# Kernel optimization log

Hardware: AMD Instinct MI355X
Metric: run time of the kernel (lower is better)

## Reference

```python
import jax, jax.numpy as jnp
import numpy as np

N = 50000; E = 800000; G = 256; F = 34; D = 128; H = 4; C = 32; L = 4
EPS = 1e-5

def _bn(x, g, b):
    # BatchNorm1d with batch statistics (train-mode math), eval dropout (identity)
    m = jnp.mean(x, 0); v = jnp.var(x, 0)
    return g * (x - m) * jax.lax.rsqrt(v + EPS) + b

def _seg_softmax(s, seg, n):
    # numerically-stable softmax over edges grouped by destination node
    m = jax.ops.segment_max(s, seg, num_segments=n)
    m = jnp.where(jnp.isfinite(m), m, 0.0)
    e = jnp.exp(s - m[seg])
    d = jax.ops.segment_sum(e, seg, num_segments=n)
    return e / (d[seg] + 1e-16)

def setup_inputs():
    key = jax.random.key(0)
    ks = iter(jax.random.split(key, 64))
    def rn(shape, s=0.05):
        return jax.random.normal(next(ks), shape, dtype=jnp.float32) * s
    inp = {}
    inp['x'] = jax.random.normal(next(ks), (N, F), dtype=jnp.float32)
    inp['edge_index'] = jax.random.randint(next(ks), (2, E), 0, N, dtype=jnp.int32)
    inp['batch'] = jnp.sort(jax.random.randint(next(ks), (N,), 0, G, dtype=jnp.int32))
    inp['emb_W'] = rn((F, D)); inp['emb_b'] = rn((D,))
    inp['emb_g'] = jnp.ones((D,)); inp['emb_be'] = jnp.zeros((D,))
    inp['gWl'] = rn((L, D, D)); inp['gWr'] = rn((L, D, D))
    inp['gbl'] = rn((L, D)); inp['gbr'] = rn((L, D))
    inp['gatt'] = rn((L, H, C)); inp['gbias'] = rn((L, D))
    inp['gg'] = jnp.ones((L, D)); inp['gbe'] = jnp.zeros((L, D))
    inp['tWq'] = rn((D, D)); inp['tWk'] = rn((D, D)); inp['tWv'] = rn((D, D)); inp['tWs'] = rn((D, D))
    inp['tbq'] = rn((D,)); inp['tbk'] = rn((D,)); inp['tbv'] = rn((D,)); inp['tbs'] = rn((D,))
    inp['tg'] = jnp.ones((D,)); inp['tbe'] = jnp.zeros((D,))
    inp['oW1'] = rn((2 * D, D)); inp['ob1'] = rn((D,))
    inp['og'] = jnp.ones((D,)); inp['obe'] = jnp.zeros((D,))
    inp['oW2'] = rn((D, D // 2)); inp['ob2'] = rn((D // 2,))
    inp['oW3'] = rn((D // 2, 1)); inp['ob3'] = rn((1,))
    return inp

def reference(x, edge_index, batch, emb_W, emb_b, emb_g, emb_be, gWl, gWr, gbl, gbr, gatt, gbias, gg, gbe, tWq, tWk, tWv, tWs, tbq, tbk, tbv, tbs, tg, tbe, oW1, ob1, og, obe, oW2, ob2, oW3, ob3):
    x = jax.nn.relu(_bn(x @ emb_W + emb_b, emb_g, emb_be))
    sl = jnp.arange(N, dtype=edge_index.dtype)
    ei = jnp.concatenate([edge_index, jnp.stack([sl, sl])], axis=1)  # GATv2 default add_self_loops=True
    src, dst = ei[0], ei[1]
    for l in range(L):  # 4 structurally identical GATv2 layers
        xl = (x @ gWl[l] + gbl[l]).reshape(N, H, C)
        xr = (x @ gWr[l] + gbr[l]).reshape(N, H, C)
        e = jax.nn.leaky_relu(xl[src] + xr[dst], 0.2)  # [E+N, H, C]
        sc = jnp.einsum('ehc,hc->eh', e, gatt[l])
        a = _seg_softmax(sc, dst, N)
        out = jax.ops.segment_sum(xl[src] * a[..., None], dst, num_segments=N).reshape(N, D) + gbias[l]
        x = x + jax.nn.relu(_bn(out, gg[l], gbe[l]))
    # TransformerConv: no self-loops by default, dot-product attention + root skip
    s2, d2 = edge_index[0], edge_index[1]
    q = (x @ tWq + tbq).reshape(N, H, C)
    k = (x @ tWk + tbk).reshape(N, H, C)
    v = (x @ tWv + tbv).reshape(N, H, C)
    sc = jnp.einsum('ehc,ehc->eh', q[d2], k[s2]) / np.float32(np.sqrt(C))
    a = _seg_softmax(sc, d2, N)
    agg = jax.ops.segment_sum(v[s2] * a[..., None], d2, num_segments=N).reshape(N, D)
    x = x + _bn(agg + x @ tWs + tbs, tg, tbe)
    # global mean + max pooling over graphs
    cnt = jax.ops.segment_sum(jnp.ones((N,), x.dtype), batch, num_segments=G)
    xm = jax.ops.segment_sum(x, batch, num_segments=G) / jnp.maximum(cnt, 1.0)[:, None]
    xx = jax.ops.segment_max(x, batch, num_segments=G)
    xx = jnp.where(jnp.isfinite(xx), xx, 0.0)  # guard empty segments
    h = jnp.concatenate([xm, xx], axis=1)
    h = jax.nn.relu(_bn(h @ oW1 + ob1, og, obe))
    h = jax.nn.relu(h @ oW2 + ob2)
    return h @ oW3 + ob3
```

## Files before the change

### kernel.cpp

```cpp
#include <hip/hip_runtime.h>
#include <hip/hip_fp16.h>

namespace {
constexpr int NN = 50000;
constexpr int NE = 800000;
constexpr int NG = 256;
constexpr int NF = 34;
constexpr int NL = 4;
constexpr int NB = (NN + 255) / 256;
constexpr int STS = 32;
}
#define EPSB 1e-5f
#define LSLOPE 0.2f
#define INV_SQRT_C 0.17677669529663687f

typedef short bf16x8 __attribute__((ext_vector_type(8)));
typedef float f32x4 __attribute__((ext_vector_type(4)));
typedef _Float16 hv2 __attribute__((ext_vector_type(2)));

static __device__ __forceinline__ short f2bf(float f) {
    unsigned int u = __float_as_uint(f);
    u = (u + 0x7fff + ((u >> 16) & 1)) >> 16;
    return (short)u;
}
static __device__ __forceinline__ unsigned fenc(float x) {
    unsigned u = __float_as_uint(x);
    return (u & 0x80000000u) ? ~u : (u | 0x80000000u);
}
static __device__ __forceinline__ float fdec(unsigned u) {
    return __uint_as_float((u & 0x80000000u) ? (u ^ 0x80000000u) : ~u);
}
static __device__ __forceinline__ float fdot2(hv2 a, hv2 b, float c) {
    return __builtin_amdgcn_fdot2(a, b, c, false);
}

__global__ __launch_bounds__(256) void k_deg(const int* __restrict__ ei,
                                             int* __restrict__ deg,
                                             int* __restrict__ rank) {
    int tid = blockIdx.x * 256 + threadIdx.x;
    const int S = (NE + 3) / 4;
    if (tid >= S) return;
#pragma unroll
    for (int k = 0; k < 4; ++k) {
        int e = tid + k * S;
        if (e < NE) rank[e] = atomicAdd(&deg[ei[NE + e]], 1);
    }
}

__global__ __launch_bounds__(256) void k_scan1(const int* __restrict__ deg, int* __restrict__ bsum) {
    __shared__ int sm[256];
    int i = blockIdx.x * 256 + threadIdx.x;
    sm[threadIdx.x] = (i < NN) ? deg[i] : 0;
    __syncthreads();
    for (int off = 128; off > 0; off >>= 1) {
        if (threadIdx.x < off) sm[threadIdx.x] += sm[threadIdx.x + off];
        __syncthreads();
    }
    if (threadIdx.x == 0) bsum[blockIdx.x] = sm[0];
}

__global__ __launch_bounds__(256) void k_scan2(const int* __restrict__ bsum,
                                               int* __restrict__ boff, int* __restrict__ rp) {
    __shared__ int sm[256];
    int t = threadIdx.x;
    int v = (t < NB) ? bsum[t] : 0;
    sm[t] = v;
    __syncthreads();
    for (int off = 1; off < 256; off <<= 1) {
        int u = (t >= off) ? sm[t - off] : 0;
        __syncthreads();
        sm[t] += u;
        __syncthreads();
    }
    if (t < NB) boff[t] = sm[t] - v;
    if (t == 255) rp[NN] = sm[255];
}

__global__ __launch_bounds__(256) void k_scan3(const int* __restrict__ deg,
                                               const int* __restrict__ boff,
                                               int* __restrict__ rp) {
    __shared__ int sm[256];
    int i = blockIdx.x * 256 + threadIdx.x;
    int t = threadIdx.x;
    int v = (i < NN) ? deg[i] : 0;
    sm[t] = v;
    __syncthreads();
    for (int off = 1; off < 256; off <<= 1) {
        int u = (t >= off) ? sm[t - off] : 0;
        __syncthreads();
        sm[t] += u;
        __syncthreads();
    }
    if (i < NN) rp[i] = boff[blockIdx.x] + sm[t] - v;
}

__global__ __launch_bounds__(256) void k_fill(const int* __restrict__ ei,
                                              const int* __restrict__ rp,
                                              const int* __restrict__ rank,
                                              int* __restrict__ esrc) {
    int tid = blockIdx.x * 256 + threadIdx.x;
    const int S = (NE + 3) / 4;
    if (tid >= S) return;
#pragma unroll
    for (int k = 0; k < 4; ++k) {
        int e = tid + k * S;
        if (e < NE) {
            int s = ei[e];
            int d = ei[NE + e];
            int p = rp[d] + rank[e];
            esrc[p] = s;
        }
    }
}

__global__ __launch_bounds__(256) void k_prep(const float* __restrict__ gWl,
                                              const float* __restrict__ gWr,
                                              const float* __restrict__ tWq,
                                              const float* __restrict__ tWk,
                                              const float* __restrict__ tWv,
                                              const float* __restrict__ tWs,
                                              short* __restrict__ dst) {
    int m = blockIdx.x;
    const float* src;
    if (m < 4) src = gWl + m * 16384;
    else if (m < 8) src = gWr + (m - 4) * 16384;
    else if (m == 8) src = tWq;
    else if (m == 9) src = tWk;
    else if (m == 10) src = tWv;
    else src = tWs;
    short* d = dst + m * 16384;
    for (int i = threadIdx.x; i < 16384; i += 256) {
        int n = i >> 7, k = i & 127;
        d[i] = f2bf(src[k * 128 + n]);
    }
}

template <int OUTH0, int OUTH1, int RES, int XOUT>
__global__ __launch_bounds__(256) void k_gemm2bn(const float* __restrict__ src,
                                                 const float* __restrict__ res,
                                                 float* __restrict__ xout,
                                                 const float* __restrict__ st,
                                                 const float* __restrict__ g,
                                                 const float* __restrict__ b,
                                                 const short* __restrict__ Wt0,
                                                 const short* __restrict__ Wt1,
                                                 const float* __restrict__ bias0,
                                                 const float* __restrict__ bias1,
                                                 void* __restrict__ out0,
                                                 void* __restrict__ out1, int nRows) {
    __shared__ short As[128 * 136];
    __shared__ short Bs[128 * 136];
    __shared__ float scsh[256];
    const float invn = 1.f / NN;
    if (threadIdx.x < 128) {
        int c = threadIdx.x;
        float s0v = 0.f, s1v = 0.f;
#pragma unroll 8
        for (int k2 = 0; k2 < STS; ++k2) {
            s0v += st[k2 * 256 + c];
            s1v += st[k2 * 256 + 128 + c];
        }
        float mean = s0v * invn;
        float var = fmaxf(s1v * invn - mean * mean, 0.f);
        float s = g[c] * rsqrtf(var + EPSB);
        scsh[c] = s;
        scsh[128 + c] = b[c] - mean * s;
    }
    {
        const int4* Wt4 = (const int4*)Wt0;
        for (int idx = threadIdx.x; idx < 2048; idx += 256) {
            int row = idx >> 4, c8 = idx & 15;
            *(int4*)&Bs[row * 136 + c8 * 8] = Wt4[idx];
        }
    }
    __syncthreads();
    int r0 = blockIdx.x * 128;
    int rows = nRows - r0; if (rows > 128) rows = 128;
    for (int idx = threadIdx.x; idx < 2048; idx += 256) {
        int r = idx >> 4, c8 = idx & 15;
        short4 sa = {0, 0, 0, 0}, sb = {0, 0, 0, 0};
        if (r < rows) {
            size_t base = (size_t)(r0 + r) * 128 + c8 * 8;
            float4 v0 = *(const float4*)&src[base];
            float4 v1 = *(const float4*)&src[base + 4];
            int c = c8 * 8;
            v0.x = fmaxf(v0.x * scsh[c + 0] + scsh[128 + c + 0], 0.f);
            v0.y = fmaxf(v0.y * scsh[c + 1] + scsh[128 + c + 1], 0.f);
            v0.z = fmaxf(v0.z * scsh[c + 2] + scsh[128 + c + 2], 0.f);
            v0.w = fmaxf(v0.w * scsh[c + 3] + scsh[128 + c + 3], 0.f);
            v1.x = fmaxf(v1.x * scsh[c + 4] + scsh[128 + c + 4], 0.f);
            v1.y = fmaxf(v1.y * scsh[c + 5] + scsh[128 + c + 5], 0.f);
            v1.z = fmaxf(v1.z * scsh[c + 6] + scsh[128 + c + 6], 0.f);
            v1.w = fmaxf(v1.w * scsh[c + 7] + scsh[128 + c + 7], 0.f);
            if (RES) {
                float4 rr0 = *(const float4*)&res[base];
                float4 rr1 = *(const float4*)&res[base + 4];
                v0.x += rr0.x; v0.y += rr0.y; v0.z += rr0.z; v0.w += rr0.w;
                v1.x += rr1.x; v1.y += rr1.y; v1.z += rr1.z; v1.w += rr1.w;
            }
            if (XOUT) {
                *(float4*)&xout[base] = v0;
                *(float4*)&xout[base + 4] = v1;
            }
            sa.x = f2bf(v0.x); sa.y = f2bf(v0.y); sa.z = f2bf(v0.z); sa.w = f2bf(v0.w);
            sb.x = f2bf(v1.x); sb.y = f2bf(v1.y); sb.z = f2bf(v1.z); sb.w = f2bf(v1.w);
        }
        *(short4*)&As[r * 136 + c8 * 8] = sa;
        *(short4*)&As[r * 136 + c8 * 8 + 4] = sb;
    }
    __syncthreads();
    int lane = threadIdx.x & 63, wave = threadIdx.x >> 6;
    int n16 = lane & 15, quad = lane >> 4;
    bf16x8 af[2][4];
#pragma unroll
    for (int rt = 0; rt < 2; ++rt)
#pragma unroll
        for (int kc = 0; kc < 4; ++kc)
            af[rt][kc] = *(const bf16x8*)&As[(wave * 32 + rt * 16 + n16) * 136 + kc * 32 + quad * 8];

    f32x4 acc[2][8];
#pragma unroll
    for (int rt = 0; rt < 2; ++rt)
#pragma unroll
        for (int ct = 0; ct < 8; ++ct) acc[rt][ct] = (f32x4){0.f, 0.f, 0.f, 0.f};
#pragma unroll
    for (int ct = 0; ct < 8; ++ct)
#pragma unroll
        for (int kc = 0; kc < 4; ++kc) {
            bf16x8 bf = *(const bf16x8*)&Bs[(ct * 16 + n16) * 136 + kc * 32 + quad * 8];
            acc[0][ct] = __builtin_amdgcn_mfma_f32_16x16x32_bf16(af[0][kc], bf, acc[0][ct], 0, 0, 0);
            acc[1][ct] = __builtin_amdgcn_mfma_f32_16x16x32_bf16(af[1][kc], bf, acc[1][ct], 0, 0, 0);
        }
#pragma unroll
    for (int ct = 0; ct < 8; ++ct) {
        int colI = ct * 16 + n16;
        float bv = bias0[colI];
#pragma unroll
        for (int rt = 0; rt < 2; ++rt)
#pragma unroll
            for (int reg = 0; reg < 4; ++reg) {
                int r = wave * 32 + rt * 16 + quad * 4 + reg;
                if (r < rows) {
                    float v = acc[rt][ct][reg] + bv;
                    if (OUTH0) ((__half*)out0)[(size_t)(r0 + r) * 128 + colI] = __float2half(v);
                    else       ((float*)out0)[(size_t)(r0 + r) * 128 + colI] = v;
                }
            }
    }
    __syncthreads();
    {
        const int4* Wt4 = (const int4*)Wt1;
        for (int idx = threadIdx.x; idx < 2048; idx += 256) {
            int row = idx >> 4, c8 = idx & 15;
            *(int4*)&Bs[row * 136 + c8 * 8] = Wt4[idx];
        }
    }
    __syncthreads();
#pragma unroll
    for (int rt = 0; rt < 2; ++rt)
#pragma unroll
        for (int ct = 0; ct < 8; ++ct) acc[rt][ct] = (f32x4){0.f, 0.f, 0.f, 0.f};
#pragma unroll
    for (int ct = 0; ct < 8; ++ct)
#pragma unroll
        for (int kc = 0; kc < 4; ++kc) {
            bf16x8 bf = *(const bf16x8*)&Bs[(ct * 16 + n16) * 136 + kc * 32 + quad * 8];
            acc[0][ct] = __builtin_amdgcn_mfma_f32_16x16x32_bf16(af[0][kc], bf, acc[0][ct], 0, 0, 0);
            acc[1][ct] = __builtin_amdgcn_mfma_f32_16x16x32_bf16(af[1][kc], bf, acc[1][ct], 0, 0, 0);
        }
#pragma unroll
    for (int ct = 0; ct < 8; ++ct) {
        int colI = ct * 16 + n16;
        float bv = bias1[colI];
#pragma unroll
        for (int rt = 0; rt < 2; ++rt)
#pragma unroll
            for (int reg = 0; reg < 4; ++reg) {
                int r = wave * 32 + rt * 16 + quad * 4 + reg;
                if (r < rows) {
                    float v = acc[rt][ct][reg] + bv;
                    if (OUTH1) ((__half*)out1)[(size_t)(r0 + r) * 128 + colI] = __float2half(v);
                    else       ((float*)out1)[(size_t)(r0 + r) * 128 + colI] = v;
                }
            }
    }
}

__global__ __launch_bounds__(256) void k_gemm4bn(const float* __restrict__ src,
                                                 const float* __restrict__ res,
                                                 float* __restrict__ xout,
                                                 const float* __restrict__ st,
                                                 const float* __restrict__ g,
                                                 const float* __restrict__ b,
                                                 const short* __restrict__ Wt,
                                                 const float* __restrict__ bq,
                                                 const float* __restrict__ bk,
                                                 const float* __restrict__ bv,
                                                 const float* __restrict__ bs,
                                                 __half* __restrict__ oq,
                                                 __half* __restrict__ ok,
                                                 __half* __restrict__ ov,
                                                 __half* __restrict__ os, int nRows) {
    __shared__ short As[128 * 136];
    __shared__ short Bs[128 * 136];
    __shared__ float scsh[256];
    const float invn = 1.f / NN;
    if (threadIdx.x < 128) {
        int c = threadIdx.x;
        float s0v = 0.f, s1v = 0.f;
#pragma unroll 8
        for (int k2 = 0; k2 < STS; ++k2) {
            s0v += st[k2 * 256 + c];
            s1v += st[k2 * 256 + 128 + c];
        }
        float mean = s0v * invn;
        float var = fmaxf(s1v * invn - mean * mean, 0.f);
        float s = g[c] * rsqrtf(var + EPSB);
        scsh[c] = s;
        scsh[128 + c] = b[c] - mean * s;
    }
    __syncthreads();
    int r0 = blockIdx.x * 128;
    int rows = nRows - r0; if (rows > 128) rows = 128;
    for (int idx = threadIdx.x; idx < 2048; idx += 256) {
        int r = idx >> 4, c8 = idx & 15;
        short4 sa = {0, 0, 0, 0}, sb = {0, 0, 0, 0};
        if (r < rows) {
            size_t base = (size_t)(r0 + r) * 128 + c8 * 8;
            float4 v0 = *(const float4*)&src[base];
            float4 v1 = *(const float4*)&src[base + 4];
            int c = c8 * 8;
            v0.x = fmaxf(v0.x * scsh[c + 0] + scsh[128 + c + 0], 0.f);
            v0.y = fmaxf(v0.y * scsh[c + 1] + scsh[128 + c + 1], 0.f);
            v0.z = fmaxf(v0.z * scsh[c + 2] + scsh[128 + c + 2], 0.f);
            v0.w = fmaxf(v0.w * scsh[c + 3] + scsh[128 + c + 3], 0.f);
            v1.x = fmaxf(v1.x * scsh[c + 4] + scsh[128 + c + 4], 0.f);
            v1.y = fmaxf(v1.y * scsh[c + 5] + scsh[128 + c + 5], 0.f);
            v1.z = fmaxf(v1.z * scsh[c + 6] + scsh[128 + c + 6], 0.f);
            v1.w = fmaxf(v1.w * scsh[c + 7] + scsh[128 + c + 7], 0.f);
            float4 rr0 = *(const float4*)&res[base];
            float4 rr1 = *(const float4*)&res[base + 4];
            v0.x += rr0.x; v0.y += rr0.y; v0.z += rr0.z; v0.w += rr0.w;
            v1.x += rr1.x; v1.y += rr1.y; v1.z += rr1.z; v1.w += rr1.w;
            *(float4*)&xout[base] = v0;
            *(float4*)&xout[base + 4] = v1;
            sa.x = f2bf(v0.x); sa.y = f2bf(v0.y); sa.z = f2bf(v0.z); sa.w = f2bf(v0.w);
            sb.x = f2bf(v1.x); sb.y = f2bf(v1.y); sb.z = f2bf(v1.z); sb.w = f2bf(v1.w);
        }
        *(short4*)&As[r * 136 + c8 * 8] = sa;
        *(short4*)&As[r * 136 + c8 * 8 + 4] = sb;
    }
    int lane = threadIdx.x & 63, wave = threadIdx.x >> 6;
    int n16 = lane & 15, quad = lane >> 4;
    __half* outs[4] = {oq, ok, ov, os};
    const float* biases[4] = {bq, bk, bv, bs};
    bf16x8 af[2][4];
    bool afLoaded = false;
    for (int m = 0; m < 4; ++m) {
        {
            const int4* Wt4 = (const int4*)(Wt + (size_t)m * 16384);
            for (int idx = threadIdx.x; idx < 2048; idx += 256) {
                int row = idx >> 4, c8 = idx & 15;
                *(int4*)&Bs[row * 136 + c8 * 8] = Wt4[idx];
            }
        }
        __syncthreads();
        if (!afLoaded) {
            afLoaded = true;
#pragma unroll
            for (int rt = 0; rt < 2; ++rt)
#pragma unroll
                for (int kc = 0; kc < 4; ++kc)
                    af[rt][kc] = *(const bf16x8*)&As[(wave * 32 + rt * 16 + n16) * 136 + kc * 32 + quad * 8];
        }
        f32x4 acc[2][8];
#pragma unroll
        for (int rt = 0; rt < 2; ++rt)
#pragma unroll
            for (int ct = 0; ct < 8; ++ct) acc[rt][ct] = (f32x4){0.f, 0.f, 0.f, 0.f};
#pragma unroll
        for (int ct = 0; ct < 8; ++ct)
#pragma unroll
            for (int kc = 0; kc < 4; ++kc) {
                bf16x8 bf = *(const bf16x8*)&Bs[(ct * 16 + n16) * 136 + kc * 32 + quad * 8];
                acc[0][ct] = __builtin_amdgcn_mfma_f32_16x16x32_bf16(af[0][kc], bf, acc[0][ct], 0, 0, 0);
                acc[1][ct] = __builtin_amdgcn_mfma_f32_16x16x32_bf16(af[1][kc], bf, acc[1][ct], 0, 0, 0);
            }
        __half* om = outs[m];
        const float* bm = biases[m];
#pragma unroll
        for (int ct = 0; ct < 8; ++ct) {
            int colI = ct * 16 + n16;
            float bv2 = bm[colI];
#pragma unroll
            for (int rt = 0; rt < 2; ++rt)
#pragma unroll
                for (int reg = 0; reg < 4; ++reg) {
                    int r = wave * 32 + rt * 16 + quad * 4 + reg;
                    if (r < rows)
                        om[(size_t)(r0 + r) * 128 + colI] = __float2half(acc[rt][ct][reg] + bv2);
                }
        }
        if (m < 3) __syncthreads();
    }
}

__global__ __launch_bounds__(256) void k_gemm_emb(const float* __restrict__ A,
                                                  const float* __restrict__ W,
                                                  const float* __restrict__ bias,
                                                  float* __restrict__ out, int nRows,
                                                  float* __restrict__ stms) {
    __shared__ float As[64 * NF];
    __shared__ float sred[256];
    int r0 = blockIdx.x * 64;
    int rows = nRows - r0; if (rows > 64) rows = 64;
    int total = rows * NF;
    for (int idx = threadIdx.x; idx < 64 * NF; idx += 256)
        As[idx] = (idx < total) ? A[(size_t)r0 * NF + idx] : 0.f;
    sred[threadIdx.x] = 0.f;
    __syncthreads();
    int tx = threadIdx.x & 31, ty = threadIdx.x >> 5;
    const float4* W4 = (const float4*)W;
    float acc[8][4];
#pragma unroll
    for (int j = 0; j < 8; ++j)
#pragma unroll
        for (int i = 0; i < 4; ++i) acc[j][i] = 0.f;
#pragma unroll 2
    for (int k = 0; k < NF; ++k) {
        float4 w = W4[k * 32 + tx];
#pragma unroll
        for (int j = 0; j < 8; ++j) {
            float a = As[(ty * 8 + j) * NF + k];
            acc[j][0] += a * w.x; acc[j][1] += a * w.y;
            acc[j][2] += a * w.z; acc[j][3] += a * w.w;
        }
    }
    float4 b = ((const float4*)bias)[tx];
    float s[4] = {0.f, 0.f, 0.f, 0.f}, ss[4] = {0.f, 0.f, 0.f, 0.f};
#pragma unroll
    for (int j = 0; j < 8; ++j) {
        int r = ty * 8 + j;
        if (r < rows) {
            float4 o = make_float4(acc[j][0] + b.x, acc[j][1] + b.y,
                                   acc[j][2] + b.z, acc[j][3] + b.w);
            ((float4*)out)[(size_t)(r0 + r) * 32 + tx] = o;
            s[0] += o.x; ss[0] += o.x * o.x;
            s[1] += o.y; ss[1] += o.y * o.y;
            s[2] += o.z; ss[2] += o.z * o.z;
            s[3] += o.w; ss[3] += o.w * o.w;
        }
    }
#pragma unroll
    for (int i = 0; i < 4; ++i) {
        atomicAdd(&sred[tx * 4 + i], s[i]);
        atomicAdd(&sred[128 + tx * 4 + i], ss[i]);
    }
    __syncthreads();
    atomicAdd(&stms[(blockIdx.x & (STS - 1)) * 256 + threadIdx.x], sred[threadIdx.x]);
}

__global__ __launch_bounds__(256) void k_gat_aggr(const __half* __restrict__ xl,
                                                  const __half* __restrict__ xr,
                                                  const float* __restrict__ att,
                                                  const float* __restrict__ gbias_l,
                                                  const int* __restrict__ rp,
                                                  const int* __restrict__ esrc,
                                                  float* __restrict__ out,
                                                  float* __restrict__ stms) {
    __shared__ float smst[256];
    smst[threadIdx.x] = 0.f;
    __syncthreads();
    int lane = threadIdx.x & 63;
    int node = blockIdx.x * 4 + (threadIdx.x >> 6);
    int q = lane >> 4;
    int l16 = lane & 15;
    int c8 = l16 * 8;
    if (node < NN) {
        float4 xrr = *(const float4*)&xr[(unsigned)node * 128u + c8];
        hv2 xrv[4] = {*(hv2*)&xrr.x, *(hv2*)&xrr.y, *(hv2*)&xrr.z, *(hv2*)&xrr.w};
        float4 atA = *(const float4*)&att[c8];
        float4 atB = *(const float4*)&att[c8 + 4];
        hv2 ath[4] = {{(_Float16)atA.x, (_Float16)atA.y}, {(_Float16)atA.z, (_Float16)atA.w},
                      {(_Float16)atB.x, (_Float16)atB.y}, {(_Float16)atB.z, (_Float16)atB.w}};
        const hv2 hz = {(_Float16)0.f, (_Float16)0.f};
        const hv2 hs = {(_Float16)LSLOPE, (_Float16)LSLOPE};
        int s0 = rp[node];
        int T = rp[node + 1] - s0 + 1;
        float a[8] = {0.f, 0.f, 0.f, 0.f, 0.f, 0.f, 0.f, 0.f};
        float l = 0.f;
        auto body = [&](int j) {
            bool self = (j == T - 1);
            int srcn = self ? node : esrc[s0 + j];
            float4 raw = *(const float4*)&xl[(unsigned)srcn * 128u + c8];
            hv2 f[4] = {*(hv2*)&raw.x, *(hv2*)&raw.y, *(hv2*)&raw.z, *(hv2*)&raw.w};
            float p = 0.f;
#pragma unroll
            for (int k = 0; k < 4; ++k) {
                hv2 e = f[k] + xrv[k];
                hv2 lk = __builtin_elementwise_max(e, hz) + hs * __builtin_elementwise_min(e, hz);
                p = fdot2(lk, ath[k], p);
            }
            p += __shfl_xor(p, 1); p += __shfl_xor(p, 2);
            float w = __expf(p);
#pragma unroll
            for (int k = 0; k < 4; ++k) {
                a[2 * k] += w * (float)f[k].x;
                a[2 * k + 1] += w * (float)f[k].y;
            }
            l += w;
        };
        int j = q;
        for (; j + 4 < T; j += 8) { body(j); body(j + 4); }
        for (; j < T; j += 4) body(j);
#pragma unroll
        for (int k = 0; k < 8; ++k) { a[k] += __shfl_xor(a[k], 16); a[k] += __shfl_xor(a[k], 32); }
        l += __shfl_xor(l, 16); l += __shfl_xor(l, 32);
        if (q == 0) {
            float inv = 1.f / (l + 1e-16f);
            float4 gb0 = *(const float4*)&gbias_l[c8];
            float4 gb1 = *(const float4*)&gbias_l[c8 + 4];
            float o[8];
            o[0] = a[0] * inv + gb0.x; o[1] = a[1] * inv + gb0.y;
            o[2] = a[2] * inv + gb0.z; o[3] = a[3] * inv + gb0.w;
            o[4] = a[4] * inv + gb1.x; o[5] = a[5] * inv + gb1.y;
            o[6] = a[6] * inv + gb1.z; o[7] = a[7] * inv + gb1.w;
            *(float4*)&out[(unsigned)node * 128u + c8] = make_float4(o[0], o[1], o[2], o[3]);
            *(float4*)&out[(unsigned)node * 128u + c8 + 4] = make_float4(o[4], o[5], o[6], o[7]);
#pragma unroll
            for (int k = 0; k < 8; ++k) {
                atomicAdd(&smst[c8 + k], o[k]);
                atomicAdd(&smst[128 + c8 + k], o[k] * o[k]);
            }
        }
    }
    __syncthreads();
    atomicAdd(&stms[(blockIdx.x & (STS - 1)) * 256 + threadIdx.x], smst[threadIdx.x]);
}

__global__ __launch_bounds__(256) void k_trans_aggr(const __half* __restrict__ qh,
                                                    const __half* __restrict__ kh,
                                                    const __half* __restrict__ vv,
                                                    const __half* __restrict__ sT,
                                                    const int* __restrict__ rp,
                                                    const int* __restrict__ esrc,
                                                    float* __restrict__ out,
                                                    float* __restrict__ stms) {
    __shared__ float smst[256];
    smst[threadIdx.x] = 0.f;
    __syncthreads();
    int lane = threadIdx.x & 63;
    int node = blockIdx.x * 4 + (threadIdx.x >> 6);
    int q = lane >> 4;
    int l16 = lane & 15;
    int c8 = l16 * 8;
    if (node < NN) {
        float4 qr = *(const float4*)&qh[(unsigned)node * 128u + c8];
        const hv2 hinv = {(_Float16)INV_SQRT_C, (_Float16)INV_SQRT_C};
        hv2 qv[4] = {(*(hv2*)&qr.x) * hinv, (*(hv2*)&qr.y) * hinv,
                     (*(hv2*)&qr.z) * hinv, (*(hv2*)&qr.w) * hinv};
        int s0 = rp[node];
        int T = rp[node + 1] - s0;
        float a[8] = {0.f, 0.f, 0.f, 0.f, 0.f, 0.f, 0.f, 0.f};
        float l = 0.f;
        auto body = [&](int j) {
            int srcn = esrc[s0 + j];
            float4 kraw = *(const float4*)&kh[(unsigned)srcn * 128u + c8];
            float4 vraw = *(const float4*)&vv[(unsigned)srcn * 128u + c8];
            hv2 kv[4] = {*(hv2*)&kraw.x, *(hv2*)&kraw.y, *(hv2*)&kraw.z, *(hv2*)&kraw.w};
            float p = 0.f;
#pragma unroll
            for (int k = 0; k < 4; ++k) p = fdot2(kv[k], qv[k], p);
            p += __shfl_xor(p, 1); p += __shfl_xor(p, 2);
            float w = __expf(p);
            hv2 vvv[4] = {*(hv2*)&vraw.x, *(hv2*)&vraw.y, *(hv2*)&vraw.z, *(hv2*)&vraw.w};
#pragma unroll
            for (int k = 0; k < 4; ++k) {
                a[2 * k] += w * (float)vvv[k].x;
                a[2 * k + 1] += w * (float)vvv[k].y;
            }
            l += w;
        };
        int j = q;
        for (; j + 4 < T; j += 8) { body(j); body(j + 4); }
        for (; j < T; j += 4) body(j);
#pragma unroll
        for (int k = 0; k < 8; ++k) { a[k] += __shfl_xor(a[k], 16); a[k] += __shfl_xor(a[k], 32); }
        l += __shfl_xor(l, 16); l += __shfl_xor(l, 32);
        if (q == 0) {
            float inv = 1.f / (l + 1e-16f);
            float4 straw = *(const float4*)&sT[(unsigned)node * 128u + c8];
            hv2 st[4] = {*(hv2*)&straw.x, *(hv2*)&straw.y, *(hv2*)&straw.z, *(hv2*)&straw.w};
            float o[8];
            o[0] = a[0] * inv + (float)st[0].x; o[1] = a[1] * inv + (float)st[0].y;
            o[2] = a[2] * inv + (float)st[1].x; o[3] = a[3] * inv + (float)st[1].y;
            o[4] = a[4] * inv + (float)st[2].x; o[5] = a[5] * inv + (float)st[2].y;
            o[6] = a[6] * inv + (float)st[3].x; o[7] = a[7] * inv + (float)st[3].y;
            *(float4*)&out[(unsigned)node * 128u + c8] = make_float4(o[0], o[1], o[2], o[3]);
            *(float4*)&out[(unsigned)node * 128u + c8 + 4] = make_float4(o[4], o[5], o[6], o[7]);
#pragma unroll
            for (int k = 0; k < 8; ++k) {
                atomicAdd(&smst[c8 + k], o[k]);
                atomicAdd(&smst[128 + c8 + k], o[k] * o[k]);
            }
        }
    }
    __syncthreads();
    atomicAdd(&stms[(blockIdx.x & (STS - 1)) * 256 + threadIdx.x], smst[threadIdx.x]);
}

__global__ __launch_bounds__(256) void k_pool_part(const float* __restrict__ src,
                                                   const float* __restrict__ res,
                                                   const float* __restrict__ st,
                                                   const float* __restrict__ g,
                                                   const float* __restrict__ b,
                                                   const int* __restrict__ batch,
                                                   float* __restrict__ psum,
                                                   unsigned* __restrict__ pmax) {
    __shared__ int bs[64];
    __shared__ float sc_sh[128], sh_sh[128];
    int r0 = blockIdx.x * 64;
    if (threadIdx.x < 64) {
        int r = r0 + threadIdx.x;
        bs[threadIdx.x] = (r < NN) ? batch[r] : -1;
    }
    const float invn = 1.f / NN;
    if (threadIdx.x < 128) {
        int c2 = threadIdx.x;
        float s0v = 0.f, s1v = 0.f;
#pragma unroll 8
        for (int k2 = 0; k2 < STS; ++k2) {
            s0v += st[k2 * 256 + c2];
            s1v += st[k2 * 256 + 128 + c2];
        }
        float mean = s0v * invn;
        float var = fmaxf(s1v * invn - mean * mean, 0.f);
        float scv = g[c2] * rsqrtf(var + EPSB);
        sc_sh[c2] = scv;
        sh_sh[c2] = b[c2] - mean * scv;
    }
    __syncthreads();
    int c = threadIdx.x & 127;
    int sub = threadIdx.x >> 7;
    float scv = sc_sh[c];
    float shv = sh_sh[c];
    int curg = -1;
    float s = 0.f, fmx = -INFINITY;
    for (int i = sub; i < 64; i += 2) {
        int r = r0 + i;
        if (r >= NN) break;
        int gr = bs[i];
        if (gr != curg) {
            if (curg >= 0) {
                atomicAdd(&psum[curg * 128 + c], s);
                atomicMax(&pmax[curg * 128 + c], fenc(fmx));
            }
            curg = gr; s = 0.f; fmx = -INFINITY;
        }
        float v = src[(size_t)r * 128 + c] * scv + shv + res[(size_t)r * 128 + c];
        s += v; fmx = fmaxf(fmx, v);
    }
    if (curg >= 0) {
        atomicAdd(&psum[curg * 128 + c], s);
        atomicMax(&pmax[curg * 128 + c], fenc(fmx));
    }
}

__global__ __launch_bounds__(128) void k_pool_head1(const float* __restrict__ psum,
                                                    const unsigned* __restrict__ pmax,
                                                    const int* __restrict__ batch,
                                                    const float* __restrict__ W,
                                                    const float* __restrict__ b,
                                                    float* __restrict__ t1,
                                                    float* __restrict__ st6) {
    __shared__ float hr[256];
    __shared__ int se[2];
    int g = blockIdx.x;
    int t = threadIdx.x;
    if (t == 0) {
        int lo = 0, hi = NN;
        while (lo < hi) { int mid = (lo + hi) >> 1; if (batch[mid] < g) lo = mid + 1; else hi = mid; }
        se[0] = lo;
        hi = NN;
        while (lo < hi) { int mid = (lo + hi) >> 1; if (batch[mid] < g + 1) lo = mid + 1; else hi = mid; }
        se[1] = lo;
    }
    __syncthreads();
    int cnt = se[1] - se[0];
    float xm = psum[g * 128 + t] / fmaxf((float)cnt, 1.f);
    float xx = (cnt > 0) ? fdec(pmax[g * 128 + t]) : 0.f;
    hr[t] = xm;
    hr[128 + t] = xx;
    __syncthreads();
    float acc = b[t];
#pragma unroll 4
    for (int k = 0; k < 256; ++k) acc += hr[k] * W[k * 128 + t];
    t1[g * 128 + t] = acc;
    atomicAdd(&st6[t], acc);
    atomicAdd(&st6[128 + t], acc * acc);
}

__global__ __launch_bounds__(64) void k_head2(const float* __restrict__ t1,
                                              const float* __restrict__ st,
                                              const float* __restrict__ og,
                                              const float* __restrict__ obe,
                                              const float* __restrict__ W2,
                                              const float* __restrict__ b2,
                                              const float* __restrict__ W3,
                                              const float* __restrict__ b3,
                                              float* __restrict__ out) {
    __shared__ float v[128];
    int row = blockIdx.x, t = threadIdx.x;
    const float invn = 1.f / NG;
#pragma unroll
    for (int half = 0; half < 2; ++half) {
        int ch = t + half * 64;
        float mean = st[ch] * invn;
        float var = fmaxf(st[128 + ch] * invn - mean * mean, 0.f);
        float scv = og[ch] * rsqrtf(var + EPSB);
        float shv = obe[ch] - mean * scv;
        float a = t1[row * 128 + ch] * scv + shv;
        v[ch] = fmaxf(a, 0.f);
    }
    __syncthreads();
    float acc = b2[t];
#pragma unroll 4
    for (int k = 0; k < 128; ++k) acc += v[k] * W2[k * 64 + t];
    float p = fmaxf(acc, 0.f) * W3[t];
    p += __shfl_xor(p, 1); p += __shfl_xor(p, 2); p += __shfl_xor(p, 4);
    p += __shfl_xor(p, 8); p += __shfl_xor(p, 16); p += __shfl_xor(p, 32);
    if (t == 0) out[row] = p + b3[0];
}

extern "C" void kernel_launch(void* const* d_in, const int* in_sizes, int n_in,
                              void* d_out, int out_size, void* d_ws, size_t ws_size,
                              hipStream_t stream) {
    const float* x_in   = (const float*)d_in[0];
    const int*   ei     = (const int*)d_in[1];
    const int*   batch  = (const int*)d_in[2];
    const float* emb_W  = (const float*)d_in[3];
    const float* emb_b  = (const float*)d_in[4];
    const float* emb_g  = (const float*)d_in[5];
    const float* emb_be = (const float*)d_in[6];
    const float* gWl    = (const float*)d_in[7];
    const float* gWr    = (const float*)d_in[8];
    const float* gbl    = (const float*)d_in[9];
    const float* gbr    = (const float*)d_in[10];
    const float* gatt   = (const float*)d_in[11];
    const float* gbias  = (const float*)d_in[12];
    const float* gg     = (const float*)d_in[13];
    const float* gbe    = (const float*)d_in[14];
    const float* tWq    = (const float*)d_in[15];
    const float* tWk    = (const float*)d_in[16];
    const float* tWv    = (const float*)d_in[17];
    const float* tWs    = (const float*)d_in[18];
    const float* tbq    = (const float*)d_in[19];
    const float* tbk    = (const float*)d_in[20];
    const float* tbv    = (const float*)d_in[21];
    const float* tbs    = (const float*)d_in[22];
    const float* tg     = (const float*)d_in[23];
    const float* tbe    = (const float*)d_in[24];
    const float* oW1    = (const float*)d_in[25];
    const float* ob1    = (const float*)d_in[26];
    const float* og     = (const float*)d_in[27];
    const float* obe    = (const float*)d_in[28];
    const float* oW2    = (const float*)d_in[29];
    const float* ob2    = (const float*)d_in[30];
    const float* oW3    = (const float*)d_in[31];
    const float* ob3    = (const float*)d_in[32];
    float* out = (float*)d_out;

    const size_t NDsz = (size_t)NN * 128;
    float* x     = (float*)d_ws;
    float* bA    = x + NDsz;
    float* bC    = bA + NDsz;
    float* stats = bC + NDsz;
    float* hpool = stats + 7 * 256;
    float* t1    = hpool + 65536;
    float* scb   = t1 + 32768;
    __half* xlh  = (__half*)(scb + (size_t)(NE + NN) * 4);
    __half* xrh  = xlh + NDsz;
    __half* vh   = xrh + NDsz;
    __half* sh   = vh + NDsz;
    short* Wt    = (short*)(sh + NDsz);
    int* deg     = (int*)(Wt + 12 * 16384);
    int* rp      = deg + NN;
    int* cursor  = rp + NN + 1;
    int2* edg    = (int2*)(cursor + NN);
    int* bsum    = (int*)(edg + NE + 64);
    int* boff    = bsum + 256;
    float* psum  = (float*)(boff + 256);
    unsigned* pmax = (unsigned*)(psum + NG * 128);
    int* rank    = (int*)scb;
    int* esrc    = (int*)edg;
    float* stms  = scb + NE;

    hipMemsetAsync(deg, 0, NN * sizeof(int), stream);
    hipMemsetAsync(stats + 6 * 256, 0, 256 * sizeof(float), stream);
    hipMemsetAsync(stms, 0, 6 * STS * 256 * sizeof(float), stream);
    hipMemsetAsync(psum, 0, NG * 128 * 2 * sizeof(float), stream);

    k_prep<<<12, 256, 0, stream>>>(gWl, gWr, tWq, tWk, tWv, tWs, Wt);

    const int S4 = (NE + 3) / 4;
    const int gQuarter = (S4 + 255) / 256;
    k_deg<<<gQuarter, 256, 0, stream>>>(ei, deg, rank);
    k_scan1<<<NB, 256, 0, stream>>>(deg, bsum);
    k_scan2<<<1, 256, 0, stream>>>(bsum, boff, rp);
    k_scan3<<<NB, 256, 0, stream>>>(deg, boff, rp);
    k_fill<<<gQuarter, 256, 0, stream>>>(ei, rp, rank, esrc);

    const int gEmb  = (NN + 63) / 64;
    const int gGemm = (NN + 127) / 128;
    const int gNode = (NN + 3) / 4;
    const int gPool = (NN + 63) / 64;
    const int REG = STS * 256;

    k_gemm_emb<<<gEmb, 256, 0, stream>>>(x_in, emb_W, emb_b, bA, NN, stms + 0 * REG);

    k_gemm2bn<1, 1, 0, 1><<<gGemm, 256, 0, stream>>>(bA, nullptr, x, stms + 0 * REG, emb_g, emb_be,
                                                     Wt + (size_t)0 * 16384, Wt + (size_t)4 * 16384,
                                                     gbl + 0 * 128, gbr + 0 * 128, xlh, xrh, NN);
    k_gat_aggr<<<gNode, 256, 0, stream>>>(xlh, xrh, gatt + 0 * 128, gbias + 0 * 128, rp, esrc, bC, stms + 1 * REG);
    k_gemm2bn<1, 1, 1, 1><<<gGemm, 256, 0, stream>>>(bC, x, bA, stms + 1 * REG, gg + 0 * 128, gbe + 0 * 128,
                                                     Wt + (size_t)1 * 16384, Wt + (size_t)5 * 16384,
                                                     gbl + 1 * 128, gbr + 1 * 128, xlh, xrh, NN);
    k_gat_aggr<<<gNode, 256, 0, stream>>>(xlh, xrh, gatt + 1 * 128, gbias + 1 * 128, rp, esrc, bC, stms + 2 * REG);
    k_gemm2bn<1, 1, 1, 1><<<gGemm, 256, 0, stream>>>(bC, bA, x, stms + 2 * REG, gg + 1 * 128, gbe + 1 * 128,
                                                     Wt + (size_t)2 * 16384, Wt + (size_t)6 * 16384,
                                                     gbl + 2 * 128, gbr + 2 * 128, xlh, xrh, NN);
    k_gat_aggr<<<gNode, 256, 0, stream>>>(xlh, xrh, gatt + 2 * 128, gbias + 2 * 128, rp, esrc, bC, stms + 3 * REG);
    k_gemm2bn<1, 1, 1, 1><<<gGemm, 256, 0, stream>>>(bC, x, bA, stms + 3 * REG, gg + 2 * 128, gbe + 2 * 128,
                                                     Wt + (size_t)3 * 16384, Wt + (size_t)7 * 16384,
                                                     gbl + 3 * 128, gbr + 3 * 128, xlh, xrh, NN);
    k_gat_aggr<<<gNode, 256, 0, stream>>>(xlh, xrh, gatt + 3 * 128, gbias + 3 * 128, rp, esrc, bC, stms + 4 * REG);

    k_gemm4bn<<<gGemm, 256, 0, stream>>>(bC, bA, x, stms + 4 * REG, gg + 3 * 128, gbe + 3 * 128,
                                         Wt + (size_t)8 * 16384, tbq, tbk, tbv, tbs,
                                         xrh, xlh, vh, sh, NN);
    k_trans_aggr<<<gNode, 256, 0, stream>>>(xrh, xlh, vh, sh, rp, esrc, bC, stms + 5 * REG);

    k_pool_part<<<gPool, 256, 0, stream>>>(bC, x, stms + 5 * REG, tg, tbe, batch, psum, pmax);
    k_pool_head1<<<NG, 128, 0, stream>>>(psum, pmax, batch, oW1, ob1, t1, stats + 6 * 256);
    k_head2<<<NG, 64, 0, stream>>>(t1, stats + 6 * 256, og, obe, oW2, ob2, oW3, ob3, out);
}
```

Measured before the change: 935.4 us.

## Split BN statistics out of aggregation kernels into a separate stats pass

Removes the per-block shared-memory atomics and global stat accumulation from the GAT and Transformer aggregation kernels, letting waves exit early and dropping the block barrier. Column sums and sums of squares are instead computed by a new k_stats kernel that rereads the fp32 aggregation output. The gather loops are also unrolled by four instead of two to put more loads in flight. The trade is an extra 25.6 MB read plus one launch per layer against cheaper, barrier-free aggregation kernels.

```diff
diff --git a/kernel.cpp b/kernel.cpp
--- a/kernel.cpp
+++ b/kernel.cpp
@@ -133,6 +133,22 @@
         int n = i >> 7, k = i & 127;
         d[i] = f2bf(src[k * 128 + n]);
     }
+}
+
+__global__ __launch_bounds__(256) void k_stats(const float* __restrict__ src, int nRows,
+                                               float* __restrict__ st) {
+    int c = threadIdx.x & 127;
+    int sub = threadIdx.x >> 7;
+    int r0 = blockIdx.x * 128;
+    int rend = r0 + 128; if (rend > nRows) rend = nRows;
+    float s = 0.f, ss = 0.f;
+    for (int r = r0 + sub; r < rend; r += 2) {
+        float v = src[(size_t)r * 128 + c];
+        s += v; ss += v * v;
+    }
+    float* dst = st + (blockIdx.x & (STS - 1)) * 256;
+    atomicAdd(&dst[c], s);
+    atomicAdd(&dst[128 + c], ss);
 }
 
 template <int OUTH0, int OUTH1, int RES, int XOUT>
@@ -466,76 +482,64 @@
                                                   const float* __restrict__ gbias_l,
                                                   const int* __restrict__ rp,
                                                   const int* __restrict__ esrc,
-                                                  float* __restrict__ out,
-                                                  float* __restrict__ stms) {
-    __shared__ float smst[256];
-    smst[threadIdx.x] = 0.f;
-    __syncthreads();
+                                                  float* __restrict__ out) {
     int lane = threadIdx.x & 63;
     int node = blockIdx.x * 4 + (threadIdx.x >> 6);
+    if (node >= NN) return;
     int q = lane >> 4;
     int l16 = lane & 15;
     int c8 = l16 * 8;
-    if (node < NN) {
-        float4 xrr = *(const float4*)&xr[(unsigned)node * 128u + c8];
-        hv2 xrv[4] = {*(hv2*)&xrr.x, *(hv2*)&xrr.y, *(hv2*)&xrr.z, *(hv2*)&xrr.w};
-        float4 atA = *(const float4*)&att[c8];
-        float4 atB = *(const float4*)&att[c8 + 4];
-        hv2 ath[4] = {{(_Float16)atA.x, (_Float16)atA.y}, {(_Float16)atA.z, (_Float16)atA.w},
-                      {(_Float16)atB.x, (_Float16)atB.y}, {(_Float16)atB.z, (_Float16)atB.w}};
-        const hv2 hz = {(_Float16)0.f, (_Float16)0.f};
-        const hv2 hs = {(_Float16)LSLOPE, (_Float16)LSLOPE};
-        int s0 = rp[node];
-        int T = rp[node + 1] - s0 + 1;
-        float a[8] = {0.f, 0.f, 0.f, 0.f, 0.f, 0.f, 0.f, 0.f};
-        float l = 0.f;
-        auto body = [&](int j) {
-            bool self = (j == T - 1);
-            int srcn = self ? node : esrc[s0 + j];
-            float4 raw = *(const float4*)&xl[(unsigned)srcn * 128u + c8];
-            hv2 f[4] = {*(hv2*)&raw.x, *(hv2*)&raw.y, *(hv2*)&raw.z, *(hv2*)&raw.w};
-            float p = 0.f;
-#pragma unroll
-            for (int k = 0; k < 4; ++k) {
-                hv2 e = f[k] + xrv[k];
-                hv2 lk = __builtin_elementwise_max(e, hz) + hs * __builtin_elementwise_min(e, hz);
-                p = fdot2(lk, ath[k], p);
-            }
-            p += __shfl_xor(p, 1); p += __shfl_xor(p, 2);
-            float w = __expf(p);
-#pragma unroll
-            for (int k = 0; k < 4; ++k) {
-                a[2 * k] += w * (float)f[k].x;
-                a[2 * k + 1] += w * (float)f[k].y;
-            }
-            l += w;
-        };
-        int j = q;
-        for (; j + 4 < T; j += 8) { body(j); body(j + 4); }
-        for (; j < T; j += 4) body(j);
-#pragma unroll
-        for (int k = 0; k < 8; ++k) { a[k] += __shfl_xor(a[k], 16); a[k] += __shfl_xor(a[k], 32); }
-        l += __shfl_xor(l, 16); l += __shfl_xor(l, 32);
-        if (q == 0) {
-            float inv = 1.f / (l + 1e-16f);
-            float4 gb0 = *(const float4*)&gbias_l[c8];
-            float4 gb1 = *(const float4*)&gbias_l[c8 + 4];
-            float o[8];
-            o[0] = a[0] * inv + gb0.x; o[1] = a[1] * inv + gb0.y;
-            o[2] = a[2] * inv + gb0.z; o[3] = a[3] * inv + gb0.w;
-            o[4] = a[4] * inv + gb1.x; o[5] = a[5] * inv + gb1.y;
-            o[6] = a[6] * inv + gb1.z; o[7] = a[7] * inv + gb1.w;
-            *(float4*)&out[(unsigned)node * 128u + c8] = make_float4(o[0], o[1], o[2], o[3]);
-            *(float4*)&out[(unsigned)node * 128u + c8 + 4] = make_float4(o[4], o[5], o[6], o[7]);
-#pragma unroll
-            for (int k = 0; k < 8; ++k) {
-                atomicAdd(&smst[c8 + k], o[k]);
-                atomicAdd(&smst[128 + c8 + k], o[k] * o[k]);
-            }
-        }
-    }
-    __syncthreads();
-    atomicAdd(&stms[(blockIdx.x & (STS - 1)) * 256 + threadIdx.x], smst[threadIdx.x]);
+    float4 xrr = *(const float4*)&xr[(unsigned)node * 128u + c8];
+    hv2 xrh[4] = {*(hv2*)&xrr.x, *(hv2*)&xrr.y, *(hv2*)&xrr.z, *(hv2*)&xrr.w};
+    float4 atA = *(const float4*)&att[c8];
+    float4 atB = *(const float4*)&att[c8 + 4];
+    hv2 ath[4] = {{(_Float16)atA.x, (_Float16)atA.y}, {(_Float16)atA.z, (_Float16)atA.w},
+                  {(_Float16)atB.x, (_Float16)atB.y}, {(_Float16)atB.z, (_Float16)atB.w}};
+    const hv2 hz = {(_Float16)0.f, (_Float16)0.f};
+    const hv2 hs = {(_Float16)LSLOPE, (_Float16)LSLOPE};
+    int s0 = rp[node];
+    int T = rp[node + 1] - s0 + 1;
+    float a[8] = {0.f, 0.f, 0.f, 0.f, 0.f, 0.f, 0.f, 0.f};
+    float l = 0.f;
+    auto body = [&](int j) {
+        bool self = (j == T - 1);
+        int srcn = self ? node : esrc[s0 + j];
+        float4 raw = *(const float4*)&xl[(unsigned)srcn * 128u + c8];
+        hv2 f[4] = {*(hv2*)&raw.x, *(hv2*)&raw.y, *(hv2*)&raw.z, *(hv2*)&raw.w};
+        float p = 0.f;
+#pragma unroll
+        for (int k = 0; k < 4; ++k) {
+            hv2 e = f[k] + xrh[k];
+            hv2 lk = __builtin_elementwise_max(e, hz) + hs * __builtin_elementwise_min(e, hz);
+            p = fdot2(lk, ath[k], p);
+        }
+        p += __shfl_xor(p, 1); p += __shfl_xor(p, 2);
+        float w = __expf(p);
+#pragma unroll
+        for (int k = 0; k < 4; ++k) {
+            a[2 * k] += w * (float)f[k].x;
+            a[2 * k + 1] += w * (float)f[k].y;
+        }
+        l += w;
+    };
+    int j = q;
+    for (; j + 12 < T; j += 16) { body(j); body(j + 4); body(j + 8); body(j + 12); }
+    for (; j + 4 < T; j += 8) { body(j); body(j + 4); }
+    for (; j < T; j += 4) body(j);
+#pragma unroll
+    for (int k = 0; k < 8; ++k) { a[k] += __shfl_xor(a[k], 16); a[k] += __shfl_xor(a[k], 32); }
+    l += __shfl_xor(l, 16); l += __shfl_xor(l, 32);
+    if (q == 0) {
+        float inv = 1.f / (l + 1e-16f);
+        float4 gb0 = *(const float4*)&gbias_l[c8];
+        float4 gb1 = *(const float4*)&gbias_l[c8 + 4];
+        float4 o0 = make_float4(a[0] * inv + gb0.x, a[1] * inv + gb0.y,
+                                a[2] * inv + gb0.z, a[3] * inv + gb0.w);
+        float4 o1 = make_float4(a[4] * inv + gb1.x, a[5] * inv + gb1.y,
+                                a[6] * inv + gb1.z, a[7] * inv + gb1.w);
+        *(float4*)&out[(unsigned)node * 128u + c8] = o0;
+        *(float4*)&out[(unsigned)node * 128u + c8 + 4] = o1;
+    }
 }
 
 __global__ __launch_bounds__(256) void k_trans_aggr(const __half* __restrict__ qh,
@@ -544,69 +548,57 @@
                                                     const __half* __restrict__ sT,
                                                     const int* __restrict__ rp,
                                                     const int* __restrict__ esrc,
-                                                    float* __restrict__ out,
-                                                    float* __restrict__ stms) {
-    __shared__ float smst[256];
-    smst[threadIdx.x] = 0.f;
-    __syncthreads();
+                                                    float* __restrict__ out) {
     int lane = threadIdx.x & 63;
     int node = blockIdx.x * 4 + (threadIdx.x >> 6);
+    if (node >= NN) return;
     int q = lane >> 4;
     int l16 = lane & 15;
     int c8 = l16 * 8;
-    if (node < NN) {
-        float4 qr = *(const float4*)&qh[(unsigned)node * 128u + c8];
-        const hv2 hinv = {(_Float16)INV_SQRT_C, (_Float16)INV_SQRT_C};
-        hv2 qv[4] = {(*(hv2*)&qr.x) * hinv, (*(hv2*)&qr.y) * hinv,
-                     (*(hv2*)&qr.z) * hinv, (*(hv2*)&qr.w) * hinv};
-        int s0 = rp[node];
-        int T = rp[node + 1] - s0;
-        float a[8] = {0.f, 0.f, 0.f, 0.f, 0.f, 0.f, 0.f, 0.f};
-        float l = 0.f;
-        auto body = [&](int j) {
-            int srcn = esrc[s0 + j];
-            float4 kraw = *(const float4*)&kh[(unsigned)srcn * 128u + c8];
-            float4 vraw = *(const float4*)&vv[(unsigned)srcn * 128u + c8];
-            hv2 kv[4] = {*(hv2*)&kraw.x, *(hv2*)&kraw.y, *(hv2*)&kraw.z, *(hv2*)&kraw.w};
-            float p = 0.f;
-#pragma unroll
-            for (int k = 0; k < 4; ++k) p = fdot2(kv[k], qv[k], p);
-            p += __shfl_xor(p, 1); p += __shfl_xor(p, 2);
-            float w = __expf(p);
-            hv2 vvv[4] = {*(hv2*)&vraw.x, *(hv2*)&vraw.y, *(hv2*)&vraw.z, *(hv2*)&vraw.w};
-#pragma unroll
-            for (int k = 0; k < 4; ++k) {
-                a[2 * k] += w * (float)vvv[k].x;
-                a[2 * k + 1] += w * (float)vvv[k].y;
-            }
-            l += w;
-        };
-        int j = q;
-        for (; j + 4 < T; j += 8) { body(j); body(j + 4); }
-        for (; j < T; j += 4) body(j);
-#pragma unroll
-        for (int k = 0; k < 8; ++k) { a[k] += __shfl_xor(a[k], 16); a[k] += __shfl_xor(a[k], 32); }
-        l += __shfl_xor(l, 16); l += __shfl_xor(l, 32);
-        if (q == 0) {
-            float inv = 1.f / (l + 1e-16f);
-            float4 straw = *(const float4*)&sT[(unsigned)node * 128u + c8];
-            hv2 st[4] = {*(hv2*)&straw.x, *(hv2*)&straw.y, *(hv2*)&straw.z, *(hv2*)&straw.w};
-            float o[8];
-            o[0] = a[0] * inv + (float)st[0].x; o[1] = a[1] * inv + (float)st[0].y;
-            o[2] = a[2] * inv + (float)st[1].x; o[3] = a[3] * inv + (float)st[1].y;
-            o[4] = a[4] * inv + (float)st[2].x; o[5] = a[5] * inv + (float)st[2].y;
-            o[6] = a[6] * inv + (float)st[3].x; o[7] = a[7] * inv + (float)st[3].y;
-            *(float4*)&out[(unsigned)node * 128u + c8] = make_float4(o[0], o[1], o[2], o[3]);
-            *(float4*)&out[(unsigned)node * 128u + c8 + 4] = make_float4(o[4], o[5], o[6], o[7]);
-#pragma unroll
-            for (int k = 0; k < 8; ++k) {
-                atomicAdd(&smst[c8 + k], o[k]);
-                atomicAdd(&smst[128 + c8 + k], o[k] * o[k]);
-            }
-        }
-    }
-    __syncthreads();
-    atomicAdd(&stms[(blockIdx.x & (STS - 1)) * 256 + threadIdx.x], smst[threadIdx.x]);
+    float4 qr = *(const float4*)&qh[(unsigned)node * 128u + c8];
+    const hv2 hinv = {(_Float16)INV_SQRT_C, (_Float16)INV_SQRT_C};
+    hv2 qv[4] = {(*(hv2*)&qr.x) * hinv, (*(hv2*)&qr.y) * hinv,
+                 (*(hv2*)&qr.z) * hinv, (*(hv2*)&qr.w) * hinv};
+    int s0 = rp[node];
+    int T = rp[node + 1] - s0;
+    float a[8] = {0.f, 0.f, 0.f, 0.f, 0.f, 0.f, 0.f, 0.f};
+    float l = 0.f;
+    auto body = [&](int j) {
+        int srcn = esrc[s0 + j];
+        float4 kraw = *(const float4*)&kh[(unsigned)srcn * 128u + c8];
+        float4 vraw = *(const float4*)&vv[(unsigned)srcn * 128u + c8];
+        hv2 kv[4] = {*(hv2*)&kraw.x, *(hv2*)&kraw.y, *(hv2*)&kraw.z, *(hv2*)&kraw.w};
+        float p = 0.f;
+#pragma unroll
+        for (int k = 0; k < 4; ++k) p = fdot2(kv[k], qv[k], p);
+        p += __shfl_xor(p, 1); p += __shfl_xor(p, 2);
+        float w = __expf(p);
+        hv2 vvv[4] = {*(hv2*)&vraw.x, *(hv2*)&vraw.y, *(hv2*)&vraw.z, *(hv2*)&vraw.w};
+#pragma unroll
+        for (int k = 0; k < 4; ++k) {
+            a[2 * k] += w * (float)vvv[k].x;
+            a[2 * k + 1] += w * (float)vvv[k].y;
+        }
+        l += w;
+    };
+    int j = q;
+    for (; j + 12 < T; j += 16) { body(j); body(j + 4); body(j + 8); body(j + 12); }
+    for (; j + 4 < T; j += 8) { body(j); body(j + 4); }
+    for (; j < T; j += 4) body(j);
+#pragma unroll
+    for (int k = 0; k < 8; ++k) { a[k] += __shfl_xor(a[k], 16); a[k] += __shfl_xor(a[k], 32); }
+    l += __shfl_xor(l, 16); l += __shfl_xor(l, 32);
+    if (q == 0) {
+        float inv = 1.f / (l + 1e-16f);
+        float4 straw = *(const float4*)&sT[(unsigned)node * 128u + c8];
+        hv2 st[4] = {*(hv2*)&straw.x, *(hv2*)&straw.y, *(hv2*)&straw.z, *(hv2*)&straw.w};
+        float4 o0 = make_float4(a[0] * inv + (float)st[0].x, a[1] * inv + (float)st[0].y,
+                                a[2] * inv + (float)st[1].x, a[3] * inv + (float)st[1].y);
+        float4 o1 = make_float4(a[4] * inv + (float)st[2].x, a[5] * inv + (float)st[2].y,
+                                a[6] * inv + (float)st[3].x, a[7] * inv + (float)st[3].y);
+        *(float4*)&out[(unsigned)node * 128u + c8] = o0;
+        *(float4*)&out[(unsigned)node * 128u + c8 + 4] = o1;
+    }
 }
 
 __global__ __launch_bounds__(256) void k_pool_part(const float* __restrict__ src,
@@ -812,6 +804,7 @@
 
     const int gEmb  = (NN + 63) / 64;
     const int gGemm = (NN + 127) / 128;
+    const int gStat = (NN + 127) / 128;
     const int gNode = (NN + 3) / 4;
     const int gPool = (NN + 63) / 64;
     const int REG = STS * 256;
@@ -821,24 +814,29 @@
     k_gemm2bn<1, 1, 0, 1><<<gGemm, 256, 0, stream>>>(bA, nullptr, x, stms + 0 * REG, emb_g, emb_be,
                                                      Wt + (size_t)0 * 16384, Wt + (size_t)4 * 16384,
                                                      gbl + 0 * 128, gbr + 0 * 128, xlh, xrh, NN);
-    k_gat_aggr<<<gNode, 256, 0, stream>>>(xlh, xrh, gatt + 0 * 128, gbias + 0 * 128, rp, esrc, bC, stms + 1 * REG);
+    k_gat_aggr<<<gNode, 256, 0, stream>>>(xlh, xrh, gatt + 0 * 128, gbias + 0 * 128, rp, esrc, bC);
+    k_stats<<<gStat, 256, 0, stream>>>(bC, NN, stms + 1 * REG);
     k_gemm2bn<1, 1, 1, 1><<<gGemm, 256, 0, stream>>>(bC, x, bA, stms + 1 * REG, gg + 0 * 128, gbe + 0 * 128,
                                                      Wt + (size_t)1 * 16384, Wt + (size_t)5 * 16384,
                                                      gbl + 1 * 128, gbr + 1 * 128, xlh, xrh, NN);
-    k_gat_aggr<<<gNode, 256, 0, stream>>>(xlh, xrh, gatt + 1 * 128, gbias + 1 * 128, rp, esrc, bC, stms + 2 * REG);
+    k_gat_aggr<<<gNode, 256, 0, stream>>>(xlh, xrh, gatt + 1 * 128, gbias + 1 * 128, rp, esrc, bC);
+    k_stats<<<gStat, 256, 0, stream>>>(bC, NN, stms + 2 * REG);
     k_gemm2bn<1, 1, 1, 1><<<gGemm, 256, 0, stream>>>(bC, bA, x, stms + 2 * REG, gg + 1 * 128, gbe + 1 * 128,
                                                      Wt + (size_t)2 * 16384, Wt + (size_t)6 * 16384,
                                                      gbl + 2 * 128, gbr + 2 * 128, xlh, xrh, NN);
-    k_gat_aggr<<<gNode, 256, 0, stream>>>(xlh, xrh, gatt + 2 * 128, gbias + 2 * 128, rp, esrc, bC, stms + 3 * REG);
+    k_gat_aggr<<<gNode, 256, 0, stream>>>(xlh, xrh, gatt + 2 * 128, gbias + 2 * 128, rp, esrc, bC);
+    k_stats<<<gStat, 256, 0, stream>>>(bC, NN, stms + 3 * REG);
     k_gemm2bn<1, 1, 1, 1><<<gGemm, 256, 0, stream>>>(bC, x, bA, stms + 3 * REG, gg + 2 * 128, gbe + 2 * 128,
                                                      Wt + (size_t)3 * 16384, Wt + (size_t)7 * 16384,
                                                      gbl + 3 * 128, gbr + 3 * 128, xlh, xrh, NN);
-    k_gat_aggr<<<gNode, 256, 0, stream>>>(xlh, xrh, gatt + 3 * 128, gbias + 3 * 128, rp, esrc, bC, stms + 4 * REG);
+    k_gat_aggr<<<gNode, 256, 0, stream>>>(xlh, xrh, gatt + 3 * 128, gbias + 3 * 128, rp, esrc, bC);
+    k_stats<<<gStat, 256, 0, stream>>>(bC, NN, stms + 4 * REG);
 
     k_gemm4bn<<<gGemm, 256, 0, stream>>>(bC, bA, x, stms + 4 * REG, gg + 3 * 128, gbe + 3 * 128,
                                          Wt + (size_t)8 * 16384, tbq, tbk, tbv, tbs,
                                          xrh, xlh, vh, sh, NN);
-    k_trans_aggr<<<gNode, 256, 0, stream>>>(xrh, xlh, vh, sh, rp, esrc, bC, stms + 5 * REG);
+    k_trans_aggr<<<gNode, 256, 0, stream>>>(xrh, xlh, vh, sh, rp, esrc, bC);
+    k_stats<<<gStat, 256, 0, stream>>>(bC, NN, stms + 5 * REG);
 
     k_pool_part<<<gPool, 256, 0, stream>>>(bC, x, stms + 5 * REG, tg, tbe, batch, psum, pmax);
     k_pool_head1<<<NG, 128, 0, stream>>>(psum, pmax, batch, oW1, ob1, t1, stats + 6 * 256);
```

Measured after the change: 821.8 us. -12.1%, faster.
